# Kernel tuning notes

Hardware: AMD Instinct MI355X
Metric: run time of the kernel (lower is better)

## Reference

```python
import jax, jax.numpy as jnp
import numpy as np

EMBED_DIM = 1024
NUM_HEADS = 16
HEAD_DIM = EMBED_DIM // NUM_HEADS


def setup_inputs() -> dict:
    key = jax.random.key(0)
    ks = jax.random.split(key, 9)
    B, S, E = 2, 2048, EMBED_DIM
    scale = 1.0 / np.sqrt(E)
    x = jax.random.normal(ks[0], (B, S, E), dtype=jnp.float32)
    Wq = jax.random.normal(ks[1], (E, E), dtype=jnp.float32) * scale
    bq = jax.random.normal(ks[2], (E,), dtype=jnp.float32) * 0.01
    Wk = jax.random.normal(ks[3], (E, E), dtype=jnp.float32) * scale
    bk = jax.random.normal(ks[4], (E,), dtype=jnp.float32) * 0.01
    Wv = jax.random.normal(ks[5], (E, E), dtype=jnp.float32) * scale
    bv = jax.random.normal(ks[6], (E,), dtype=jnp.float32) * 0.01
    Wo = jax.random.normal(ks[7], (E, E), dtype=jnp.float32) * scale
    bo = jax.random.normal(ks[8], (E,), dtype=jnp.float32) * 0.01
    return {"x": x, "Wq": Wq, "bq": bq, "Wk": Wk, "bk": bk,
            "Wv": Wv, "bv": bv, "Wo": Wo, "bo": bo}


def reference(x, Wq, bq, Wk, bk, Wv, bv, Wo, bo):
    B, S, E = x.shape
    H, D = NUM_HEADS, HEAD_DIM
    # projections (torch Linear: x @ W.T + b), reshape to (B, H, S, D)
    q = (x @ Wq.T + bq).reshape(B, S, H, D).transpose(0, 2, 1, 3)
    k = (x @ Wk.T + bk).reshape(B, S, H, D).transpose(0, 2, 1, 3)
    v = (x @ Wv.T + bv).reshape(B, S, H, D).transpose(0, 2, 1, 3)
    softmax_scale = 1.0 / np.sqrt(D)
    # (B, H, S, S) scores, causal mask, stable softmax
    scores = softmax_scale * jnp.einsum('bhsd,bhtd->bhst', q, k)
    causal = jnp.tril(jnp.ones((S, S), dtype=bool))  # True = keep
    scores = jnp.where(causal, scores, -jnp.inf)
    attn = jax.nn.softmax(scores, axis=-1)
    out = jnp.einsum('bhst,bhtd->bhsd', attn, v)  # (B, H, S, D)
    out = out.transpose(0, 2, 1, 3).reshape(B, S, E)
    return out @ Wo.T + bo
```

## Files before the change

### kernel.cpp

```cpp
#include <hip/hip_runtime.h>
#include <cstdint>
#include <cstddef>

#define SEQ   2048
#define BATCH 2
#define EMB   1024
#define NH    16
#define HD    64
#define MTOT  (BATCH * SEQ)
#define NX    (MTOT * EMB)
#define NW    (EMB * EMB)
#define QS    3072

typedef __bf16 bf16_t;
typedef __bf16 bf16x2 __attribute__((ext_vector_type(2)));
typedef __bf16 bf16x4 __attribute__((ext_vector_type(4)));
typedef __bf16 bf16x8 __attribute__((ext_vector_type(8)));
typedef float  f32x4  __attribute__((ext_vector_type(4)));
typedef float  f32x16 __attribute__((ext_vector_type(16)));

typedef __attribute__((address_space(1))) const void* as1cv;
typedef __attribute__((address_space(3))) void*       as3v;

__device__ __forceinline__ void async_cp16(const void* g, void* l) {
  __builtin_amdgcn_global_load_lds((as1cv)g, (as3v)l, 16, 0, 0);
}

__device__ __forceinline__ f32x16 mfma32(bf16x8 a, bf16x8 b, f32x16 c) {
  return __builtin_amdgcn_mfma_f32_32x32x16_bf16(a, b, c, 0, 0, 0);
}

__device__ __forceinline__ uint32_t pk2(float a, float b) {
  bf16x2 t; t[0] = (bf16_t)a; t[1] = (bf16_t)b;
  return __builtin_bit_cast(uint32_t, t);
}
__device__ __forceinline__ bf16x8 mk_frag(uint32_t x, uint32_t y,
                                          uint32_t z, uint32_t w) {
  uint4 u; u.x = x; u.y = y; u.z = z; u.w = w;
  return __builtin_bit_cast(bf16x8, u);
}

__global__ __launch_bounds__(256) void cvt_all(
    const float* __restrict__ x,  const float* __restrict__ wq,
    const float* __restrict__ wk, const float* __restrict__ wv,
    const float* __restrict__ wo,
    bf16_t* __restrict__ xb,  bf16_t* __restrict__ wqb,
    bf16_t* __restrict__ wkb, bf16_t* __restrict__ wvb,
    bf16_t* __restrict__ wob) {
  long e = ((long)blockIdx.x * 256 + threadIdx.x) * 4;
  const float* s; bf16_t* d; long off;
  if (e < NX) { s = x; d = xb; off = e; }
  else {
    long e2 = e - NX;
    int w = (int)(e2 >> 20);
    off = e2 & (NW - 1);
    s = (w == 0) ? wq : (w == 1) ? wk : (w == 2) ? wv : wo;
    d = (w == 0) ? wqb : (w == 1) ? wkb : (w == 2) ? wvb : wob;
  }
  float4 v = *(const float4*)(s + off);
  bf16x4 o;
  o[0] = (bf16_t)v.x; o[1] = (bf16_t)v.y; o[2] = (bf16_t)v.z; o[3] = (bf16_t)v.w;
  *(bf16x4*)(d + off) = o;
}

__global__ __launch_bounds__(256) void vtrans(const bf16_t* __restrict__ QKV,
                                              bf16_t* __restrict__ VT) {
  const int hb = blockIdx.x;
  const int sb = blockIdx.y;
  const int h = hb & 15, b = hb >> 4;
  const int t = threadIdx.x;
  __shared__ __align__(16) bf16_t Ts[64 * 72];
  const bf16_t* Vp = QKV + ((size_t)(b * SEQ + sb * 64)) * QS + 2048 + h * HD;
  const int sr = t >> 4, d0 = (t & 15) * 4;
#pragma unroll
  for (int i = 0; i < 4; ++i) {
    bf16x4 v = *(const bf16x4*)(Vp + (size_t)(sr + 16 * i) * QS + d0);
    *(bf16x4*)&Ts[(sr + 16 * i) * 72 + d0] = v;
  }
  __syncthreads();
  const int d = t >> 2, tc = (t & 3) * 16;
  __align__(16) bf16_t out[16];
#pragma unroll
  for (int j = 0; j < 16; ++j) out[j] = Ts[(tc + j) * 72 + d];
  bf16_t* dst = VT + ((size_t)hb * HD + d) * SEQ + sb * 64 + tc;
  *(uint4*)(dst)     = *(uint4*)&out[0];
  *(uint4*)(dst + 8) = *(uint4*)&out[8];
}

template <typename OT, int BN, int CS>
__global__ __launch_bounds__(256) void gemm_f(
    const bf16_t* __restrict__ A, const bf16_t* __restrict__ Bw,
    const float* __restrict__ b0, const float* __restrict__ b1,
    const float* __restrict__ b2, OT* __restrict__ C) {
  constexpr int K = EMB, BK = 64;
  __shared__ __align__(16) bf16_t As[128 * BK];
  __shared__ __align__(16) bf16_t Bs[BN * BK];

  const int tid  = threadIdx.x;
  const int lane = tid & 63;
  const int wave = tid >> 6;
  const int l31  = lane & 31;
  const int hi   = lane >> 5;
  const int wm   = (wave >> 1) * 64;
  const int wn   = (wave & 1) * (BN / 2);
  const int m0   = blockIdx.y * 128;
  const int n0   = blockIdx.x * BN;

  const float* bias = (n0 < 1024) ? b0 : ((n0 < 2048) ? b1 : b2);

  const int row0 = tid >> 3, slot = tid & 7;
  const bf16_t* gA[4];
  const bf16_t* gB[BN / 32];
#pragma unroll
  for (int i = 0; i < 4; ++i)
    gA[i] = A + (size_t)(m0 + row0 + 32 * i) * K + (slot ^ (row0 & 7)) * 8;
#pragma unroll
  for (int i = 0; i < BN / 32; ++i)
    gB[i] = Bw + (size_t)(n0 + row0 + 32 * i) * K + (slot ^ (row0 & 7)) * 8;

  f32x16 acc[2][BN / 64] = {};
  const int sw = l31 & 7;

  for (int kk = 0; kk < K; kk += BK) {
#pragma unroll
    for (int i = 0; i < 4; ++i)
      async_cp16(gA[i] + kk, &As[(tid + 256 * i) * 8]);
#pragma unroll
    for (int i = 0; i < BN / 32; ++i)
      async_cp16(gB[i] + kk, &Bs[(tid + 256 * i) * 8]);
    __syncthreads();

#pragma unroll
    for (int ks = 0; ks < 4; ++ks) {
      const int js = ((ks * 2 + hi) ^ sw) * 8;
      bf16x8 af[2], bfr[BN / 64];
#pragma unroll
      for (int i = 0; i < 2; ++i)
        af[i] = *(const bf16x8*)&As[(wm + i * 32 + l31) * BK + js];
#pragma unroll
      for (int j = 0; j < BN / 64; ++j)
        bfr[j] = *(const bf16x8*)&Bs[(wn + j * 32 + l31) * BK + js];
#pragma unroll
      for (int i = 0; i < 2; ++i)
#pragma unroll
        for (int j = 0; j < BN / 64; ++j)
          acc[i][j] = mfma32(af[i], bfr[j], acc[i][j]);
    }
    __syncthreads();
  }

#pragma unroll
  for (int i = 0; i < 2; ++i)
#pragma unroll
    for (int j = 0; j < BN / 64; ++j) {
      const int col = n0 + wn + j * 32 + l31;
      const float bv = bias[col & 1023];
#pragma unroll
      for (int r = 0; r < 16; ++r) {
        const int row = m0 + wm + i * 32 + (r & 3) + 8 * (r >> 2) + 4 * hi;
        C[(size_t)row * CS + col] = (OT)(acc[i][j][r] + bv);
      }
    }
}

__global__ __launch_bounds__(256, 3) void attn128(
    const bf16_t* __restrict__ QKVg, const bf16_t* __restrict__ VTg,
    bf16_t* __restrict__ Og) {
  const int hb  = blockIdx.x;
  const int y   = blockIdx.y;
  const int s   = (y < 8) ? (15 - y) : (y - 8);
  const int h   = hb & 15, b = hb >> 4;
  const int tid = threadIdx.x;
  const int lane = tid & 63, wave = tid >> 6;
  const int l31 = lane & 31, hi = lane >> 5;
  const bool h0 = (hi == 0);

  __shared__ __align__(16) bf16_t Ks[2][64 * 72];
  __shared__ __align__(16) bf16_t VsT[2][64 * 72];
  __shared__ __align__(16) bf16_t Qs[128 * 64];

  const size_t base = ((size_t)b * SEQ) * QS + (size_t)h * HD;
  const bf16_t* Qb  = QKVg + base;
  const bf16_t* Kp  = QKVg + base + 1024;
  const bf16_t* VTp = VTg + (size_t)hb * HD * SEQ;

  const int kr0r = tid >> 3, kcol = (tid & 7) * 8;
  const int kr1r = kr0r + 32;
  const int lo0 = kr0r * 72 + kcol;
  const int lo1 = lo0 + 32 * 72;

  const int q0  = s * 128;
  const int nit = 2 * s + 2;
  const bf16_t* Qp = Qb + (size_t)q0 * QS;

  uint4 kr0 = *(const uint4*)(Kp + (size_t)kr0r * QS + kcol);
  uint4 kr1 = *(const uint4*)(Kp + (size_t)kr1r * QS + kcol);
  uint4 vr0 = *(const uint4*)(VTp + (size_t)kr0r * SEQ + kcol);
  uint4 vr1 = *(const uint4*)(VTp + (size_t)kr1r * SEQ + kcol);

#pragma unroll
  for (int i = 0; i < 4; ++i) {
    const int c = tid + 256 * i;
    *(uint4*)&Qs[(c >> 3) * 64 + (c & 7) * 8] =
        *(const uint4*)(Qp + (size_t)(c >> 3) * QS + (c & 7) * 8);
  }
  __syncthreads();

  bf16x8 qf[4];
#pragma unroll
  for (int kk = 0; kk < 4; ++kk)
    qf[kk] = *(const bf16x8*)&Qs[(32 * wave + l31) * 64 + kk * 16 + hi * 8];

  f32x16 acc_t0 = {}, acc_t1 = {};
  float lsum = 0.f;

  for (int it = 0; it < nit; ++it) {
    bf16_t* Kc = &Ks[it & 1][0];
    bf16_t* Vc = &VsT[it & 1][0];
    *(uint4*)&Kc[lo0] = kr0;
    *(uint4*)&Kc[lo1] = kr1;
    *(uint4*)&Vc[lo0] = vr0;
    *(uint4*)&Vc[lo1] = vr1;
    __syncthreads();

    if (it + 1 < nit) {
      const bf16_t* Kn  = Kp + (size_t)(it + 1) * 64 * QS;
      const bf16_t* VTn = VTp + (it + 1) * 64;
      kr0 = *(const uint4*)(Kn + (size_t)kr0r * QS + kcol);
      kr1 = *(const uint4*)(Kn + (size_t)kr1r * QS + kcol);
      vr0 = *(const uint4*)(VTn + (size_t)kr0r * SEQ + kcol);
      vr1 = *(const uint4*)(VTn + (size_t)kr1r * SEQ + kcol);
    }

    const bool active = (64 * it <= q0 + 32 * wave + 31);
    if (active) {
      f32x16 s0 = {}, s1 = {};
#pragma unroll
      for (int kk = 0; kk < 4; ++kk) {
        const bf16x8 kf0 = *(const bf16x8*)&Kc[l31 * 72 + kk * 16 + hi * 8];
        const bf16x8 kf1 =
            *(const bf16x8*)&Kc[(32 + l31) * 72 + kk * 16 + hi * 8];
        s0 = mfma32(kf0, qf[kk], s0);
        s1 = mfma32(kf1, qf[kk], s1);
      }

      constexpr float SC2 = 0.18033688011112042f;
      if (it >= nit - 2) {
        const int qg = q0 + 32 * wave + l31;
        const int k0 = 64 * it + 4 * hi;
#pragma unroll
        for (int r = 0; r < 16; ++r) {
          const int key = k0 + (r & 3) + 8 * (r >> 2);
          float p0 = exp2f(__builtin_fmaf(s0[r], SC2, -8.f));
          float p1 = exp2f(__builtin_fmaf(s1[r], SC2, -8.f));
          if (key > qg) p0 = 0.f;
          if (key + 32 > qg) p1 = 0.f;
          s0[r] = p0; s1[r] = p1;
          lsum += p0 + p1;
        }
      } else {
#pragma unroll
        for (int r = 0; r < 16; ++r) {
          const float p0 = exp2f(__builtin_fmaf(s0[r], SC2, -8.f));
          const float p1 = exp2f(__builtin_fmaf(s1[r], SC2, -8.f));
          s0[r] = p0; s1[r] = p1;
          lsum += p0 + p1;
        }
      }

      bf16x8 pf[4];
#pragma unroll
      for (int kk = 0; kk < 4; ++kk) {
        const f32x16& g = (kk < 2) ? s0 : s1;
        const int bir = 8 * (kk & 1);
        const uint32_t PL0 = pk2(g[bir + 0], g[bir + 1]);
        const uint32_t PL1 = pk2(g[bir + 2], g[bir + 3]);
        const uint32_t PH0 = pk2(g[bir + 4], g[bir + 5]);
        const uint32_t PH1 = pk2(g[bir + 6], g[bir + 7]);
        const uint32_t XL0 = (uint32_t)__shfl_xor((int)PL0, 32, 64);
        const uint32_t XL1 = (uint32_t)__shfl_xor((int)PL1, 32, 64);
        const uint32_t XH0 = (uint32_t)__shfl_xor((int)PH0, 32, 64);
        const uint32_t XH1 = (uint32_t)__shfl_xor((int)PH1, 32, 64);
        pf[kk] = h0 ? mk_frag(PL0, PL1, XL0, XL1)
                    : mk_frag(XH0, XH1, PH0, PH1);
      }

#pragma unroll
      for (int kk = 0; kk < 4; ++kk) {
        const bf16x8 vf0 = *(const bf16x8*)&Vc[l31 * 72 + kk * 16 + hi * 8];
        const bf16x8 vf1 =
            *(const bf16x8*)&Vc[(32 + l31) * 72 + kk * 16 + hi * 8];
        acc_t0 = mfma32(vf0, pf[kk], acc_t0);
        acc_t1 = mfma32(vf1, pf[kk], acc_t1);
      }
    }
  }

  const float lt = lsum + __shfl_xor(lsum, 32, 64);
  const float inv = 1.f / lt;
  bf16_t* Ow = &Qs[(32 * wave) * 64];
#pragma unroll
  for (int a = 0; a < 4; ++a)
#pragma unroll
    for (int c = 0; c < 4; c += 2) {
      const int r = 4 * a + c;
      const int d = c + 8 * a + 4 * hi;
      *(uint32_t*)&Ow[l31 * 64 + d] =
          pk2(acc_t0[r] * inv, acc_t0[r + 1] * inv);
      *(uint32_t*)&Ow[l31 * 64 + d + 32] =
          pk2(acc_t1[r] * inv, acc_t1[r + 1] * inv);
    }
  bf16_t* Op = Og + ((size_t)b * SEQ + q0 + 32 * wave) * EMB + (size_t)h * HD;
#pragma unroll
  for (int i = 0; i < 4; ++i) {
    const int id = lane + 64 * i;
    const int row = id >> 3, col8 = (id & 7) * 8;
    *(uint4*)(Op + (size_t)row * EMB + col8) =
        *(const uint4*)&Ow[row * 64 + col8];
  }
}

extern "C" void kernel_launch(void* const* d_in, const int* in_sizes, int n_in,
                              void* d_out, int out_size, void* d_ws,
                              size_t ws_size, hipStream_t stream) {
  const float* x  = (const float*)d_in[0];
  const float* Wq = (const float*)d_in[1];
  const float* bq = (const float*)d_in[2];
  const float* Wk = (const float*)d_in[3];
  const float* bk = (const float*)d_in[4];
  const float* Wv = (const float*)d_in[5];
  const float* bv = (const float*)d_in[6];
  const float* Wo = (const float*)d_in[7];
  const float* bo = (const float*)d_in[8];
  float* out = (float*)d_out;

  char* p = (char*)d_ws;
  bf16_t* xb   = (bf16_t*)p; p += (size_t)NX * 2;
  bf16_t* wqb  = (bf16_t*)p; p += (size_t)NW * 2;
  bf16_t* wkb  = (bf16_t*)p; p += (size_t)NW * 2;
  bf16_t* wvb  = (bf16_t*)p; p += (size_t)NW * 2;
  bf16_t* wob  = (bf16_t*)p; p += (size_t)NW * 2;
  bf16_t* qkvb = (bf16_t*)p; p += (size_t)NX * 3 * 2;
  bf16_t* ab   = (bf16_t*)p; p += (size_t)NX * 2;
  bf16_t* vtb  = xb;

  const int ntot = NX + 4 * NW;
  cvt_all<<<dim3(ntot / 4 / 256), 256, 0, stream>>>(
      x, Wq, Wk, Wv, Wo, xb, wqb, wkb, wvb, wob);

  gemm_f<bf16_t, 128, QS><<<dim3(QS / 128, MTOT / 128), 256, 0, stream>>>(
      xb, wqb, bq, bk, bv, qkvb);

  vtrans<<<dim3(BATCH * NH, SEQ / 64), 256, 0, stream>>>(qkvb, vtb);

  attn128<<<dim3(BATCH * NH, SEQ / 128), 256, 0, stream>>>(qkvb, vtb, ab);

  gemm_f<float, 64, EMB><<<dim3(EMB / 64, MTOT / 128), 256, 0, stream>>>(
      ab, wob, bo, bo, bo, out);
}
```

Before: 187.4 us.

## Split attention KV by parity across blocks, pair q-tiles, add combine kernel

The attention kernel now splits the key/value tiles into even and odd halves across a new grid dimension. Each block processes two paired query tiles (s and 15-s) to balance the causal work, and writes unnormalized partial outputs plus row sums. A new combine kernel adds the two partials and normalizes them. The output projection GEMM also moves to 64x64 tiles to launch more blocks. The aim is better load balance and more parallelism in attention, at the cost of an extra output buffer, an extra kernel launch, and extra memory traffic. This works without a running max because the softmax uses a fixed offset.

```diff
diff --git a/kernel.cpp b/kernel.cpp
--- a/kernel.cpp
+++ b/kernel.cpp
@@ -16,7 +16,6 @@
 typedef __bf16 bf16x2 __attribute__((ext_vector_type(2)));
 typedef __bf16 bf16x4 __attribute__((ext_vector_type(4)));
 typedef __bf16 bf16x8 __attribute__((ext_vector_type(8)));
-typedef float  f32x4  __attribute__((ext_vector_type(4)));
 typedef float  f32x16 __attribute__((ext_vector_type(16)));
 
 typedef __attribute__((address_space(1))) const void* as1cv;
@@ -87,13 +86,13 @@
   *(uint4*)(dst + 8) = *(uint4*)&out[8];
 }
 
-template <typename OT, int BN, int CS>
+template <typename OT, int BM, int BN, int CS>
 __global__ __launch_bounds__(256) void gemm_f(
     const bf16_t* __restrict__ A, const bf16_t* __restrict__ Bw,
     const float* __restrict__ b0, const float* __restrict__ b1,
     const float* __restrict__ b2, OT* __restrict__ C) {
   constexpr int K = EMB, BK = 64;
-  __shared__ __align__(16) bf16_t As[128 * BK];
+  __shared__ __align__(16) bf16_t As[BM * BK];
   __shared__ __align__(16) bf16_t Bs[BN * BK];
 
   const int tid  = threadIdx.x;
@@ -101,29 +100,29 @@
   const int wave = tid >> 6;
   const int l31  = lane & 31;
   const int hi   = lane >> 5;
-  const int wm   = (wave >> 1) * 64;
+  const int wm   = (wave >> 1) * (BM / 2);
   const int wn   = (wave & 1) * (BN / 2);
-  const int m0   = blockIdx.y * 128;
+  const int m0   = blockIdx.y * BM;
   const int n0   = blockIdx.x * BN;
 
   const float* bias = (n0 < 1024) ? b0 : ((n0 < 2048) ? b1 : b2);
 
   const int row0 = tid >> 3, slot = tid & 7;
-  const bf16_t* gA[4];
+  const bf16_t* gA[BM / 32];
   const bf16_t* gB[BN / 32];
 #pragma unroll
-  for (int i = 0; i < 4; ++i)
+  for (int i = 0; i < BM / 32; ++i)
     gA[i] = A + (size_t)(m0 + row0 + 32 * i) * K + (slot ^ (row0 & 7)) * 8;
 #pragma unroll
   for (int i = 0; i < BN / 32; ++i)
     gB[i] = Bw + (size_t)(n0 + row0 + 32 * i) * K + (slot ^ (row0 & 7)) * 8;
 
-  f32x16 acc[2][BN / 64] = {};
+  f32x16 acc[BM / 64][BN / 64] = {};
   const int sw = l31 & 7;
 
   for (int kk = 0; kk < K; kk += BK) {
 #pragma unroll
-    for (int i = 0; i < 4; ++i)
+    for (int i = 0; i < BM / 32; ++i)
       async_cp16(gA[i] + kk, &As[(tid + 256 * i) * 8]);
 #pragma unroll
     for (int i = 0; i < BN / 32; ++i)
@@ -133,15 +132,15 @@
 #pragma unroll
     for (int ks = 0; ks < 4; ++ks) {
       const int js = ((ks * 2 + hi) ^ sw) * 8;
-      bf16x8 af[2], bfr[BN / 64];
-#pragma unroll
-      for (int i = 0; i < 2; ++i)
+      bf16x8 af[BM / 64], bfr[BN / 64];
+#pragma unroll
+      for (int i = 0; i < BM / 64; ++i)
         af[i] = *(const bf16x8*)&As[(wm + i * 32 + l31) * BK + js];
 #pragma unroll
       for (int j = 0; j < BN / 64; ++j)
         bfr[j] = *(const bf16x8*)&Bs[(wn + j * 32 + l31) * BK + js];
 #pragma unroll
-      for (int i = 0; i < 2; ++i)
+      for (int i = 0; i < BM / 64; ++i)
 #pragma unroll
         for (int j = 0; j < BN / 64; ++j)
           acc[i][j] = mfma32(af[i], bfr[j], acc[i][j]);
@@ -150,7 +149,7 @@
   }
 
 #pragma unroll
-  for (int i = 0; i < 2; ++i)
+  for (int i = 0; i < BM / 64; ++i)
 #pragma unroll
     for (int j = 0; j < BN / 64; ++j) {
       const int col = n0 + wn + j * 32 + l31;
@@ -165,10 +164,11 @@
 
 __global__ __launch_bounds__(256, 3) void attn128(
     const bf16_t* __restrict__ QKVg, const bf16_t* __restrict__ VTg,
-    bf16_t* __restrict__ Og) {
+    bf16_t* __restrict__ Oe, bf16_t* __restrict__ Oo,
+    float* __restrict__ Lg) {
   const int hb  = blockIdx.x;
   const int y   = blockIdx.y;
-  const int s   = (y < 8) ? (15 - y) : (y - 8);
+  const int par = blockIdx.z;
   const int h   = hb & 15, b = hb >> 4;
   const int tid = threadIdx.x;
   const int lane = tid & 63, wave = tid >> 6;
@@ -183,141 +183,165 @@
   const bf16_t* Qb  = QKVg + base;
   const bf16_t* Kp  = QKVg + base + 1024;
   const bf16_t* VTp = VTg + (size_t)hb * HD * SEQ;
+  bf16_t* Opar = par ? Oo : Oe;
+  float*  Lp   = Lg + par * (32 * 2048) + hb * 2048;
 
   const int kr0r = tid >> 3, kcol = (tid & 7) * 8;
   const int kr1r = kr0r + 32;
   const int lo0 = kr0r * 72 + kcol;
   const int lo1 = lo0 + 32 * 72;
 
-  const int q0  = s * 128;
-  const int nit = 2 * s + 2;
-  const bf16_t* Qp = Qb + (size_t)q0 * QS;
-
-  uint4 kr0 = *(const uint4*)(Kp + (size_t)kr0r * QS + kcol);
-  uint4 kr1 = *(const uint4*)(Kp + (size_t)kr1r * QS + kcol);
-  uint4 vr0 = *(const uint4*)(VTp + (size_t)kr0r * SEQ + kcol);
-  uint4 vr1 = *(const uint4*)(VTp + (size_t)kr1r * SEQ + kcol);
-
-#pragma unroll
-  for (int i = 0; i < 4; ++i) {
-    const int c = tid + 256 * i;
-    *(uint4*)&Qs[(c >> 3) * 64 + (c & 7) * 8] =
-        *(const uint4*)(Qp + (size_t)(c >> 3) * QS + (c & 7) * 8);
-  }
-  __syncthreads();
-
-  bf16x8 qf[4];
-#pragma unroll
-  for (int kk = 0; kk < 4; ++kk)
-    qf[kk] = *(const bf16x8*)&Qs[(32 * wave + l31) * 64 + kk * 16 + hi * 8];
-
-  f32x16 acc_t0 = {}, acc_t1 = {};
-  float lsum = 0.f;
-
-  for (int it = 0; it < nit; ++it) {
-    bf16_t* Kc = &Ks[it & 1][0];
-    bf16_t* Vc = &VsT[it & 1][0];
-    *(uint4*)&Kc[lo0] = kr0;
-    *(uint4*)&Kc[lo1] = kr1;
-    *(uint4*)&Vc[lo0] = vr0;
-    *(uint4*)&Vc[lo1] = vr1;
+  for (int ph = 0; ph < 2; ++ph) {
+    const int s   = ph ? (15 - y) : y;
+    const int q0  = s * 128;
+    const int n   = s + 1;
+    const bf16_t* Qp = Qb + (size_t)q0 * QS;
+
+    uint4 kr0 = *(const uint4*)(Kp + (size_t)(par * 64 + kr0r) * QS + kcol);
+    uint4 kr1 = *(const uint4*)(Kp + (size_t)(par * 64 + kr1r) * QS + kcol);
+    uint4 vr0 = *(const uint4*)(VTp + (size_t)kr0r * SEQ + par * 64 + kcol);
+    uint4 vr1 = *(const uint4*)(VTp + (size_t)kr1r * SEQ + par * 64 + kcol);
+
     __syncthreads();
-
-    if (it + 1 < nit) {
-      const bf16_t* Kn  = Kp + (size_t)(it + 1) * 64 * QS;
-      const bf16_t* VTn = VTp + (it + 1) * 64;
-      kr0 = *(const uint4*)(Kn + (size_t)kr0r * QS + kcol);
-      kr1 = *(const uint4*)(Kn + (size_t)kr1r * QS + kcol);
-      vr0 = *(const uint4*)(VTn + (size_t)kr0r * SEQ + kcol);
-      vr1 = *(const uint4*)(VTn + (size_t)kr1r * SEQ + kcol);
-    }
-
-    const bool active = (64 * it <= q0 + 32 * wave + 31);
-    if (active) {
-      f32x16 s0 = {}, s1 = {};
-#pragma unroll
-      for (int kk = 0; kk < 4; ++kk) {
-        const bf16x8 kf0 = *(const bf16x8*)&Kc[l31 * 72 + kk * 16 + hi * 8];
-        const bf16x8 kf1 =
-            *(const bf16x8*)&Kc[(32 + l31) * 72 + kk * 16 + hi * 8];
-        s0 = mfma32(kf0, qf[kk], s0);
-        s1 = mfma32(kf1, qf[kk], s1);
+#pragma unroll
+    for (int i = 0; i < 4; ++i) {
+      const int c = tid + 256 * i;
+      *(uint4*)&Qs[(c >> 3) * 64 + (c & 7) * 8] =
+          *(const uint4*)(Qp + (size_t)(c >> 3) * QS + (c & 7) * 8);
+    }
+    __syncthreads();
+
+    bf16x8 qf[4];
+#pragma unroll
+    for (int kk = 0; kk < 4; ++kk)
+      qf[kk] = *(const bf16x8*)&Qs[(32 * wave + l31) * 64 + kk * 16 + hi * 8];
+
+    f32x16 acc_t0 = {}, acc_t1 = {};
+    float lsum = 0.f;
+
+    for (int it = 0; it < n; ++it) {
+      const int kt = par + 2 * it;
+      bf16_t* Kc = &Ks[it & 1][0];
+      bf16_t* Vc = &VsT[it & 1][0];
+      *(uint4*)&Kc[lo0] = kr0;
+      *(uint4*)&Kc[lo1] = kr1;
+      *(uint4*)&Vc[lo0] = vr0;
+      *(uint4*)&Vc[lo1] = vr1;
+      __syncthreads();
+
+      if (it + 1 < n) {
+        const bf16_t* Kn  = Kp + (size_t)(kt + 2) * 64 * QS;
+        const bf16_t* VTn = VTp + (kt + 2) * 64;
+        kr0 = *(const uint4*)(Kn + (size_t)kr0r * QS + kcol);
+        kr1 = *(const uint4*)(Kn + (size_t)kr1r * QS + kcol);
+        vr0 = *(const uint4*)(VTn + (size_t)kr0r * SEQ + kcol);
+        vr1 = *(const uint4*)(VTn + (size_t)kr1r * SEQ + kcol);
       }
 
-      constexpr float SC2 = 0.18033688011112042f;
-      if (it >= nit - 2) {
-        const int qg = q0 + 32 * wave + l31;
-        const int k0 = 64 * it + 4 * hi;
-#pragma unroll
-        for (int r = 0; r < 16; ++r) {
-          const int key = k0 + (r & 3) + 8 * (r >> 2);
-          float p0 = exp2f(__builtin_fmaf(s0[r], SC2, -8.f));
-          float p1 = exp2f(__builtin_fmaf(s1[r], SC2, -8.f));
-          if (key > qg) p0 = 0.f;
-          if (key + 32 > qg) p1 = 0.f;
-          s0[r] = p0; s1[r] = p1;
-          lsum += p0 + p1;
+      const bool active = (64 * kt <= q0 + 32 * wave + 31);
+      if (active) {
+        f32x16 s0 = {}, s1 = {};
+#pragma unroll
+        for (int kk = 0; kk < 4; ++kk) {
+          const bf16x8 kf0 = *(const bf16x8*)&Kc[l31 * 72 + kk * 16 + hi * 8];
+          const bf16x8 kf1 =
+              *(const bf16x8*)&Kc[(32 + l31) * 72 + kk * 16 + hi * 8];
+          s0 = mfma32(kf0, qf[kk], s0);
+          s1 = mfma32(kf1, qf[kk], s1);
         }
-      } else {
-#pragma unroll
-        for (int r = 0; r < 16; ++r) {
-          const float p0 = exp2f(__builtin_fmaf(s0[r], SC2, -8.f));
-          const float p1 = exp2f(__builtin_fmaf(s1[r], SC2, -8.f));
-          s0[r] = p0; s1[r] = p1;
-          lsum += p0 + p1;
+
+        constexpr float SC2 = 0.18033688011112042f;
+        if (it == n - 1) {
+          const int qg = q0 + 32 * wave + l31;
+          const int k0 = 64 * kt + 4 * hi;
+#pragma unroll
+          for (int r = 0; r < 16; ++r) {
+            const int key = k0 + (r & 3) + 8 * (r >> 2);
+            float p0 = exp2f(__builtin_fmaf(s0[r], SC2, -8.f));
+            float p1 = exp2f(__builtin_fmaf(s1[r], SC2, -8.f));
+            if (key > qg) p0 = 0.f;
+            if (key + 32 > qg) p1 = 0.f;
+            s0[r] = p0; s1[r] = p1;
+            lsum += p0 + p1;
+          }
+        } else {
+#pragma unroll
+          for (int r = 0; r < 16; ++r) {
+            const float p0 = exp2f(__builtin_fmaf(s0[r], SC2, -8.f));
+            const float p1 = exp2f(__builtin_fmaf(s1[r], SC2, -8.f));
+            s0[r] = p0; s1[r] = p1;
+            lsum += p0 + p1;
+          }
+        }
+
+        bf16x8 pf[4];
+#pragma unroll
+        for (int kk = 0; kk < 4; ++kk) {
+          const f32x16& g = (kk < 2) ? s0 : s1;
+          const int bir = 8 * (kk & 1);
+          const uint32_t PL0 = pk2(g[bir + 0], g[bir + 1]);
+          const uint32_t PL1 = pk2(g[bir + 2], g[bir + 3]);
+          const uint32_t PH0 = pk2(g[bir + 4], g[bir + 5]);
+          const uint32_t PH1 = pk2(g[bir + 6], g[bir + 7]);
+          const uint32_t XL0 = (uint32_t)__shfl_xor((int)PL0, 32, 64);
+          const uint32_t XL1 = (uint32_t)__shfl_xor((int)PL1, 32, 64);
+          const uint32_t XH0 = (uint32_t)__shfl_xor((int)PH0, 32, 64);
+          const uint32_t XH1 = (uint32_t)__shfl_xor((int)PH1, 32, 64);
+          pf[kk] = h0 ? mk_frag(PL0, PL1, XL0, XL1)
+                      : mk_frag(XH0, XH1, PH0, PH1);
+        }
+
+#pragma unroll
+        for (int kk = 0; kk < 4; ++kk) {
+          const bf16x8 vf0 = *(const bf16x8*)&Vc[l31 * 72 + kk * 16 + hi * 8];
+          const bf16x8 vf1 =
+              *(const bf16x8*)&Vc[(32 + l31) * 72 + kk * 16 + hi * 8];
+          acc_t0 = mfma32(vf0, pf[kk], acc_t0);
+          acc_t1 = mfma32(vf1, pf[kk], acc_t1);
         }
       }
-
-      bf16x8 pf[4];
-#pragma unroll
-      for (int kk = 0; kk < 4; ++kk) {
-        const f32x16& g = (kk < 2) ? s0 : s1;
-        const int bir = 8 * (kk & 1);
-        const uint32_t PL0 = pk2(g[bir + 0], g[bir + 1]);
-        const uint32_t PL1 = pk2(g[bir + 2], g[bir + 3]);
-        const uint32_t PH0 = pk2(g[bir + 4], g[bir + 5]);
-        const uint32_t PH1 = pk2(g[bir + 6], g[bir + 7]);
-        const uint32_t XL0 = (uint32_t)__shfl_xor((int)PL0, 32, 64);
-        const uint32_t XL1 = (uint32_t)__shfl_xor((int)PL1, 32, 64);
-        const uint32_t XH0 = (uint32_t)__shfl_xor((int)PH0, 32, 64);
-        const uint32_t XH1 = (uint32_t)__shfl_xor((int)PH1, 32, 64);
-        pf[kk] = h0 ? mk_frag(PL0, PL1, XL0, XL1)
-                    : mk_frag(XH0, XH1, PH0, PH1);
+    }
+
+    const float lt = lsum + __shfl_xor(lsum, 32, 64);
+    if (h0) Lp[q0 + 32 * wave + l31] = lt;
+    bf16_t* Ow = &Qs[(32 * wave) * 64];
+#pragma unroll
+    for (int a = 0; a < 4; ++a)
+#pragma unroll
+      for (int c = 0; c < 4; c += 2) {
+        const int r = 4 * a + c;
+        const int d = c + 8 * a + 4 * hi;
+        *(uint32_t*)&Ow[l31 * 64 + d]      = pk2(acc_t0[r], acc_t0[r + 1]);
+        *(uint32_t*)&Ow[l31 * 64 + d + 32] = pk2(acc_t1[r], acc_t1[r + 1]);
       }
-
-#pragma unroll
-      for (int kk = 0; kk < 4; ++kk) {
-        const bf16x8 vf0 = *(const bf16x8*)&Vc[l31 * 72 + kk * 16 + hi * 8];
-        const bf16x8 vf1 =
-            *(const bf16x8*)&Vc[(32 + l31) * 72 + kk * 16 + hi * 8];
-        acc_t0 = mfma32(vf0, pf[kk], acc_t0);
-        acc_t1 = mfma32(vf1, pf[kk], acc_t1);
-      }
+    bf16_t* Op = Opar + ((size_t)b * SEQ + q0 + 32 * wave) * EMB
+                      + (size_t)h * HD;
+#pragma unroll
+    for (int i = 0; i < 4; ++i) {
+      const int id = lane + 64 * i;
+      const int row = id >> 3, col8 = (id & 7) * 8;
+      *(uint4*)(Op + (size_t)row * EMB + col8) =
+          *(const uint4*)&Ow[row * 64 + col8];
     }
   }
-
-  const float lt = lsum + __shfl_xor(lsum, 32, 64);
-  const float inv = 1.f / lt;
-  bf16_t* Ow = &Qs[(32 * wave) * 64];
-#pragma unroll
-  for (int a = 0; a < 4; ++a)
-#pragma unroll
-    for (int c = 0; c < 4; c += 2) {
-      const int r = 4 * a + c;
-      const int d = c + 8 * a + 4 * hi;
-      *(uint32_t*)&Ow[l31 * 64 + d] =
-          pk2(acc_t0[r] * inv, acc_t0[r + 1] * inv);
-      *(uint32_t*)&Ow[l31 * 64 + d + 32] =
-          pk2(acc_t1[r] * inv, acc_t1[r + 1] * inv);
-    }
-  bf16_t* Op = Og + ((size_t)b * SEQ + q0 + 32 * wave) * EMB + (size_t)h * HD;
-#pragma unroll
-  for (int i = 0; i < 4; ++i) {
-    const int id = lane + 64 * i;
-    const int row = id >> 3, col8 = (id & 7) * 8;
-    *(uint4*)(Op + (size_t)row * EMB + col8) =
-        *(const uint4*)&Ow[row * 64 + col8];
-  }
+}
+
+__global__ __launch_bounds__(256) void combine(
+    bf16_t* __restrict__ Oe, const bf16_t* __restrict__ Oo,
+    const float* __restrict__ Lg) {
+  const long idx = ((long)blockIdx.x * 256 + threadIdx.x) * 8;
+  const int row = (int)(idx >> 10);
+  const int col = (int)(idx & 1023);
+  const int b = row >> 11, sg = row & 2047, h = col >> 6;
+  const int li = (b * 16 + h) * 2048 + sg;
+  const float inv = 1.f / (Lg[li] + Lg[32 * 2048 + li]);
+  const bf16x8 e = *(const bf16x8*)(Oe + idx);
+  const bf16x8 o = *(const bf16x8*)(Oo + idx);
+  bf16x8 rr;
+#pragma unroll
+  for (int u = 0; u < 8; ++u)
+    rr[u] = (bf16_t)(((float)e[u] + (float)o[u]) * inv);
+  *(bf16x8*)(Oe + idx) = rr;
 }
 
 extern "C" void kernel_launch(void* const* d_in, const int* in_sizes, int n_in,
@@ -342,19 +366,25 @@
   bf16_t* wob  = (bf16_t*)p; p += (size_t)NW * 2;
   bf16_t* qkvb = (bf16_t*)p; p += (size_t)NX * 3 * 2;
   bf16_t* ab   = (bf16_t*)p; p += (size_t)NX * 2;
+  bf16_t* oob  = (bf16_t*)p; p += (size_t)NX * 2;
+  float*  lb   = (float*)p;  p += (size_t)2 * 32 * 2048 * 4;
   bf16_t* vtb  = xb;
 
   const int ntot = NX + 4 * NW;
   cvt_all<<<dim3(ntot / 4 / 256), 256, 0, stream>>>(
       x, Wq, Wk, Wv, Wo, xb, wqb, wkb, wvb, wob);
 
-  gemm_f<bf16_t, 128, QS><<<dim3(QS / 128, MTOT / 128), 256, 0, stream>>>(
-      xb, wqb, bq, bk, bv, qkvb);
+  gemm_f<bf16_t, 128, 128, QS>
+      <<<dim3(QS / 128, MTOT / 128), 256, 0, stream>>>(
+          xb, wqb, bq, bk, bv, qkvb);
 
   vtrans<<<dim3(BATCH * NH, SEQ / 64), 256, 0, stream>>>(qkvb, vtb);
 
-  attn128<<<dim3(BATCH * NH, SEQ / 128), 256, 0, stream>>>(qkvb, vtb, ab);
-
-  gemm_f<float, 64, EMB><<<dim3(EMB / 64, MTOT / 128), 256, 0, stream>>>(
-      ab, wob, bo, bo, bo, out);
-}
+  attn128<<<dim3(BATCH * NH, 8, 2), 256, 0, stream>>>(qkvb, vtb, ab, oob, lb);
+
+  combine<<<dim3(NX / 8 / 256), 256, 0, stream>>>(ab, oob, lb);
+
+  gemm_f<float, 64, 64, EMB>
+      <<<dim3(EMB / 64, MTOT / 64), 256, 0, stream>>>(
+          ab, wob, bo, bo, bo, out);
+}
```

Result: slower. 191.8 us (+2.4%).
